# Kernel tuning notes

Measured on AMD Instinct MI355X. Metric: run time of the kernel, lower is better.

## Reference

```python
import jax, jax.numpy as jnp
import numpy as np

N_HEADS = 16
NEG_BIAS = -1e9


def setup_inputs() -> dict:
    key = jax.random.key(0)
    kq, kk, kv = jax.random.split(key, 3)
    B, S, D = 2, 2048, 1024
    queries = jax.random.normal(kq, (B, S, D), dtype=jnp.float32)
    keys = jax.random.normal(kk, (B, S, D), dtype=jnp.float32)
    values = jax.random.normal(kv, (B, S, D), dtype=jnp.float32)
    # causal mask [B, S, S]: True = attend allowed
    mask = jnp.broadcast_to(jnp.tril(jnp.ones((S, S), dtype=bool)), (B, S, S))
    return {"queries": queries, "keys": keys, "values": values, "mask": mask}


def reference(queries, keys, values, mask):
    B, S, D = queries.shape
    H = N_HEADS
    dh = D // H

    def split_heads(t):  # [B,S,D] -> [B,H,S,dh]
        return t.reshape(B, -1, H, dh).transpose(0, 2, 1, 3)

    q = split_heads(queries)
    k = split_heads(keys)
    v = split_heads(values)

    # scaled dot-product similarity: [B,H,Sq,Sk]
    sim = jnp.einsum('bhqd,bhkd->bhqk', q, k) / jnp.sqrt(jnp.asarray(dh, q.dtype))

    # additive mask bias (mask rank 3 -> broadcast over heads)
    bias = NEG_BIAS * (~mask).astype(sim.dtype)  # [B,Sq,Sk]
    masked = sim + bias[:, None, :, :]

    # stable softmax (original subtracts row max then softmaxes)
    weights = jax.nn.softmax(masked, axis=-1)

    # dropout is identity at inference (rate=None -> 0)
    out = jnp.einsum('bhqk,bhkd->bhqd', weights, v)

    # combine heads: [B,H,S,dh] -> [B,S,D]
    out = out.transpose(0, 2, 1, 3).reshape(B, S, D)
    return out
```

## Files before the change

### kernel.cpp

```cpp
#include <hip/hip_runtime.h>

#define B_ 2
#define S_ 2048
#define D_ 1024
#define H_ 16
#define DH 64
#define KB 64
#define SCALE_LOG2 0.18033688011112042f
#define THR 11.0f

typedef _Float16 f16x8 __attribute__((ext_vector_type(8)));
typedef _Float16 f16x4 __attribute__((ext_vector_type(4)));
typedef __fp16   h16x2 __attribute__((ext_vector_type(2)));
typedef float f32x4 __attribute__((ext_vector_type(4)));


__device__ __forceinline__ f16x8 cvt8(const float* x, float s) {
  f16x8 r;
#pragma unroll
  for (int i = 0; i < 4; ++i) {
    h16x2 p = __builtin_amdgcn_cvt_pkrtz(x[2*i] * s, x[2*i+1] * s);
    r[2*i] = (_Float16)p[0]; r[2*i+1] = (_Float16)p[1];
  }
  return r;
}

__global__ __launch_bounds__(256) void mha_fwd(
    const float* __restrict__ qg, const float* __restrict__ kg,
    const float* __restrict__ vg, float* __restrict__ out)
{
  __shared__ __align__(16) _Float16 lds_k[KB * DH];
  __shared__ __align__(16) _Float16 lds_v[DH * KB];

  int bx  = blockIdx.x;
  int xcd = bx & 7;
  int L   = bx >> 3;
  int bh  = xcd * 4 + (L & 3);
  int qb  = 31 - (L >> 2);
  int h = bh & 15;
  int b = bh >> 4;

  int tid  = threadIdx.x;
  int wid  = tid >> 6;
  int lane = tid & 63;
  int n    = lane & 15;
  int g    = lane >> 4;

  const float* qbase = qg + (size_t)b * S_ * D_ + h * DH;
  const float* kbase = kg + (size_t)b * S_ * D_ + h * DH;
  const float* vbase = vg + (size_t)b * S_ * D_ + h * DH;

  const int skey  = tid >> 2;
  const int spart = tid & 3;
  const int vdh   = tid & 63;
  const int vkq   = tid >> 6;

  float4 kf[4];
  float  vf[16];

  auto load_tile = [&](int kt) {
    const float* kp = kbase + (size_t)(kt * KB + skey) * D_ + spart * 16;
#pragma unroll
    for (int i = 0; i < 4; ++i) kf[i] = ((const float4*)kp)[i];
    const float* vp = vbase + (size_t)(kt * KB + vkq * 16) * D_ + vdh;
#pragma unroll
    for (int j = 0; j < 16; ++j) vf[j] = vp[(size_t)j * D_];
  };

  auto store_tile = [&]() {
    const float* kfl = (const float*)kf;
    f16x8 h0 = cvt8(kfl, 1.f), h1 = cvt8(kfl + 8, 1.f);
    int c0 = spart * 2;
    char* kb_ = (char*)lds_k;
    *(f16x8*)(kb_ + skey * 128 + (((c0    ) ^ (skey & 7)) << 4)) = h0;
    *(f16x8*)(kb_ + skey * 128 + (((c0 + 1) ^ (skey & 7)) << 4)) = h1;
    f16x8 v0 = cvt8(vf, 1.f), v1 = cvt8(vf + 8, 1.f);
    int kb8 = vkq * 2;
    _Float16* vt = lds_v + vdh * 64;
    *(f16x8*)(vt + (((kb8    ) ^ (vdh & 7)) << 3)) = v0;
    *(f16x8*)(vt + (((kb8 + 1) ^ (vdh & 7)) << 3)) = v1;
  };

  const int nkt  = qb + 1;
  const int qrow = qb * 64 + wid * 16;

  f16x8 bq[2];
  {
    const float* qp = qbase + (size_t)(qrow + n) * D_ + g * 8;
    float x[16];
#pragma unroll
    for (int c = 0; c < 2; ++c) {
      *(float4*)(x + 8*c)     = *(const float4*)(qp + c * 32);
      *(float4*)(x + 8*c + 4) = *(const float4*)(qp + c * 32 + 4);
    }
    bq[0] = cvt8(x, SCALE_LOG2);
    bq[1] = cvt8(x + 8, SCALE_LOG2);
  }

  f32x4 o_acc[4] = {};
  float m_run = 0.f, l_run = 0.f;

  load_tile(0);

  for (int kt = 0; kt < nkt; ++kt) {
    __syncthreads();
    store_tile();
    __syncthreads();
    if (kt + 1 < nkt) load_tile(kt + 1);

    __builtin_amdgcn_s_setprio(1);
    const char* kb_ = (const char*)lds_k;
    f32x4 sc[4] = {};
#pragma unroll
    for (int t = 0; t < 4; ++t) {
      int keyl = t * 16 + n;
#pragma unroll
      for (int c = 0; c < 2; ++c) {
        int off = keyl * 128 + (((c * 4 + g) ^ (keyl & 7)) << 4);
        f16x8 ak = *(f16x8*)(kb_ + off);
        sc[t] = __builtin_amdgcn_mfma_f32_16x16x32_f16(ak, bq[c], sc[t], 0, 0, 0);
      }
    }

    if (kt == nkt - 1) {
      int q = qrow + n;
#pragma unroll
      for (int t = 0; t < 4; ++t)
#pragma unroll
        for (int r = 0; r < 4; ++r) {
          int key = kt * KB + t * 16 + 4 * g + r;
          if (key > q) sc[t][r] = -1e30f;
        }
    }

    float mxt[4];
#pragma unroll
    for (int t = 0; t < 4; ++t)
      mxt[t] = fmaxf(fmaxf(sc[t][0], sc[t][1]), fmaxf(sc[t][2], sc[t][3]));
    float mx = fmaxf(fmaxf(mxt[0], mxt[1]), fmaxf(mxt[2], mxt[3]));
    mx = fmaxf(mx, __shfl_xor(mx, 16, 64));
    mx = fmaxf(mx, __shfl_xor(mx, 32, 64));

    float s = 0.f;
#pragma unroll
    for (int t = 0; t < 4; ++t) {
      f32x4 p = sc[t];
#pragma unroll
      for (int r = 0; r < 4; ++r) p[r] = exp2f(p[r] - m_run);
      sc[t] = p;
      s += (p[0] + p[1]) + (p[2] + p[3]);
    }

    if (!__all(mx <= m_run + THR)) {
      float mnew  = fmaxf(m_run, mx);
      float alpha = exp2f(m_run - mnew);
#pragma unroll
      for (int t = 0; t < 4; ++t)
#pragma unroll
        for (int r = 0; r < 4; ++r) sc[t][r] *= alpha;
      s *= alpha;
      l_run *= alpha;
      m_run = mnew;
      float ar[4];
#pragma unroll
      for (int r = 0; r < 4; ++r) ar[r] = __shfl(alpha, 4 * g + r, 64);
#pragma unroll
      for (int nt = 0; nt < 4; ++nt)
#pragma unroll
        for (int r = 0; r < 4; ++r) o_acc[nt][r] *= ar[r];
    }
    l_run += s;

    f16x4 pa[4];
#pragma unroll
    for (int u = 0; u < 4; ++u) {
      h16x2 p0 = __builtin_amdgcn_cvt_pkrtz(sc[u][0], sc[u][1]);
      h16x2 p1 = __builtin_amdgcn_cvt_pkrtz(sc[u][2], sc[u][3]);
      f16x4 p4;
      p4[0] = (_Float16)p0[0]; p4[1] = (_Float16)p0[1];
      p4[2] = (_Float16)p1[0]; p4[3] = (_Float16)p1[1];
      pa[u] = p4;
    }

#pragma unroll
    for (int u = 0; u < 4; ++u) {
#pragma unroll
      for (int nt = 0; nt < 4; ++nt) {
        int dhv = nt * 16 + n;
        int off = dhv * 64 + ((((2 * u + (g >> 1)) ^ (n & 7))) << 3) + ((g & 1) << 2);
        f16x4 bv = *(f16x4*)(lds_v + off);
        o_acc[nt] = __builtin_amdgcn_mfma_f32_16x16x16f16(pa[u], bv, o_acc[nt], 0, 0, 0);
      }
    }
    __builtin_amdgcn_s_setprio(0);
  }

  float lsum = l_run;
  lsum += __shfl_xor(lsum, 16, 64);
  lsum += __shfl_xor(lsum, 32, 64);
  float linv[4];
#pragma unroll
  for (int r = 0; r < 4; ++r) linv[r] = 1.0f / __shfl(lsum, 4 * g + r, 64);

  float* ob = out + ((size_t)b * S_ + qrow) * D_ + h * DH;
#pragma unroll
  for (int r = 0; r < 4; ++r) {
    float* op = ob + (size_t)(4 * g + r) * D_ + n;
#pragma unroll
    for (int nt = 0; nt < 4; ++nt)
      op[nt * 16] = o_acc[nt][r] * linv[r];
  }
}

extern "C" void kernel_launch(void* const* d_in, const int* in_sizes, int n_in,
                              void* d_out, int out_size, void* d_ws, size_t ws_size,
                              hipStream_t stream) {
  const float* q = (const float*)d_in[0];
  const float* k = (const float*)d_in[1];
  const float* v = (const float*)d_in[2];
  float* out = (float*)d_out;
  dim3 grid(1024);
  mha_fwd<<<grid, 256, 0, stream>>>(q, k, v, out);
}
```

Baseline: 154.4 us.

## Split long causal query blocks across key chunks with atomic-counter merge

Each query block's key range is cut into chunks of 8 tiles, so the grid grows from 1024 to 2560 blocks and the causal triangle's work is spread more evenly. Each chunk writes a partial output in fp16 plus its row max and sum to workspace. The last-arriving block, found with an atomic counter, merges the partials with a log-sum-exp rescale. This adds an extra counter-zeroing launch, workspace traffic and fp16 rounding of the partials. The original single-pass kernel is kept as a fallback when workspace is too small.

```diff
diff --git a/kernel.cpp b/kernel.cpp
--- a/kernel.cpp
+++ b/kernel.cpp
@@ -9,6 +9,11 @@
 #define SCALE_LOG2 0.18033688011112042f
 #define THR 11.0f
 
+#define CHUNK 8
+#define PSTRIDE 8704
+#define NSLOTS 2304
+#define WS_NEED (4096 + NSLOTS * PSTRIDE)
+
 typedef _Float16 f16x8 __attribute__((ext_vector_type(8)));
 typedef _Float16 f16x4 __attribute__((ext_vector_type(4)));
 typedef __fp16   h16x2 __attribute__((ext_vector_type(2)));
@@ -25,18 +30,29 @@
   return r;
 }
 
-__global__ __launch_bounds__(256) void mha_fwd(
+__global__ void zero_cnt(int* c) {
+  int i = blockIdx.x * 256 + threadIdx.x;
+  if (i < 1024) c[i] = 0;
+}
+
+__global__ __launch_bounds__(256) void mha_fwd_split(
     const float* __restrict__ qg, const float* __restrict__ kg,
-    const float* __restrict__ vg, float* __restrict__ out)
+    const float* __restrict__ vg, float* __restrict__ out,
+    char* __restrict__ wsp)
 {
   __shared__ __align__(16) _Float16 lds_k[KB * DH];
   __shared__ __align__(16) _Float16 lds_v[DH * KB];
+  __shared__ int s_last;
 
   int bx  = blockIdx.x;
-  int xcd = bx & 7;
-  int L   = bx >> 3;
-  int bh  = xcd * 4 + (L & 3);
-  int qb  = 31 - (L >> 2);
+  int L   = (bx & 7) * 320 + (bx >> 3);
+  int bh  = L / 80;
+  int idx = 79 - (L % 80);
+  int qb, ch, nch;
+  if (idx < 8)       { qb = idx;                 ch = 0;              nch = 1; }
+  else if (idx < 24) { qb = 8  + ((idx - 8) >> 1);  ch = (idx - 8) & 1;  nch = 2; }
+  else if (idx < 48) { qb = 16 + (idx - 24) / 3;    ch = (idx - 24) % 3; nch = 3; }
+  else               { qb = 24 + ((idx - 48) >> 2); ch = (idx - 48) & 3; nch = 4; }
   int h = bh & 15;
   int b = bh >> 4;
 
@@ -82,6 +98,8 @@
   };
 
   const int nkt  = qb + 1;
+  const int k0   = ch * CHUNK;
+  const int kend = min(k0 + CHUNK, nkt);
   const int qrow = qb * 64 + wid * 16;
 
   f16x8 bq[2];
@@ -100,13 +118,13 @@
   f32x4 o_acc[4] = {};
   float m_run = 0.f, l_run = 0.f;
 
-  load_tile(0);
-
-  for (int kt = 0; kt < nkt; ++kt) {
+  load_tile(k0);
+
+  for (int kt = k0; kt < kend; ++kt) {
     __syncthreads();
     store_tile();
     __syncthreads();
-    if (kt + 1 < nkt) load_tile(kt + 1);
+    if (kt + 1 < kend) load_tile(kt + 1);
 
     __builtin_amdgcn_s_setprio(1);
     const char* kb_ = (const char*)lds_k;
@@ -122,7 +140,7 @@
       }
     }
 
-    if (kt == nkt - 1) {
+    if (kt == qb) {
       int q = qrow + n;
 #pragma unroll
       for (int t = 0; t < 4; ++t)
@@ -202,6 +220,249 @@
 #pragma unroll
   for (int r = 0; r < 4; ++r) linv[r] = 1.0f / __shfl(lsum, 4 * g + r, 64);
 
+  if (nch == 1) {
+    float* ob = out + ((size_t)b * S_ + qrow) * D_ + h * DH;
+#pragma unroll
+    for (int r = 0; r < 4; ++r) {
+      float* op = ob + (size_t)(4 * g + r) * D_ + n;
+#pragma unroll
+      for (int nt = 0; nt < 4; ++nt)
+        op[nt * 16] = o_acc[nt][r] * linv[r];
+    }
+    return;
+  }
+
+  int off_q = (qb < 16) ? (qb - 8) * 2 : (qb < 24) ? 16 + (qb - 16) * 3 : 40 + (qb - 24) * 4;
+  int slot0 = bh * 72 + off_q;
+  char* pbase = wsp + 4096 + (size_t)(slot0 + ch) * PSTRIDE;
+  {
+    _Float16* Op = (_Float16*)pbase;
+#pragma unroll
+    for (int r = 0; r < 4; ++r) {
+      int prow = wid * 16 + 4 * g + r;
+#pragma unroll
+      for (int nt = 0; nt < 4; ++nt)
+        Op[prow * 64 + nt * 16 + n] = (_Float16)(o_acc[nt][r] * linv[r]);
+    }
+    if (lane < 16) {
+      *(float*)(pbase + 8192 + (wid * 16 + n) * 4) = m_run;
+      *(float*)(pbase + 8448 + (wid * 16 + n) * 4) = lsum;
+    }
+  }
+  __threadfence();
+  __syncthreads();
+  int* cnt = (int*)wsp + bh * 24 + (qb - 8);
+  if (tid == 0) s_last = (atomicAdd(cnt, 1) == nch - 1);
+  __syncthreads();
+  if (!s_last) return;
+  __threadfence();
+
+  {
+    const char* pb0 = wsp + 4096 + (size_t)slot0 * PSTRIDE;
+    int row = tid >> 2;
+    int c0  = (tid & 3) * 16;
+    float mi[4], li[4], M = -1e30f;
+    for (int i = 0; i < nch; ++i) {
+      const char* p = pb0 + (size_t)i * PSTRIDE;
+      mi[i] = *(const float*)(p + 8192 + row * 4);
+      li[i] = *(const float*)(p + 8448 + row * 4);
+      M = fmaxf(M, mi[i]);
+    }
+    float o[16];
+#pragma unroll
+    for (int j = 0; j < 16; ++j) o[j] = 0.f;
+    float wsum = 0.f;
+    for (int i = 0; i < nch; ++i) {
+      float w = li[i] * exp2f(mi[i] - M);
+      wsum += w;
+      const _Float16* Op = (const _Float16*)(pb0 + (size_t)i * PSTRIDE) + row * 64 + c0;
+#pragma unroll
+      for (int j = 0; j < 16; ++j) o[j] += w * (float)Op[j];
+    }
+    float inv = 1.0f / wsum;
+    float* op = out + ((size_t)b * S_ + qb * 64 + row) * D_ + h * DH + c0;
+#pragma unroll
+    for (int j = 0; j < 16; ++j) op[j] = o[j] * inv;
+  }
+}
+
+__global__ __launch_bounds__(256) void mha_fwd(
+    const float* __restrict__ qg, const float* __restrict__ kg,
+    const float* __restrict__ vg, float* __restrict__ out)
+{
+  __shared__ __align__(16) _Float16 lds_k[KB * DH];
+  __shared__ __align__(16) _Float16 lds_v[DH * KB];
+
+  int bx  = blockIdx.x;
+  int xcd = bx & 7;
+  int L   = bx >> 3;
+  int bh  = xcd * 4 + (L & 3);
+  int qb  = 31 - (L >> 2);
+  int h = bh & 15;
+  int b = bh >> 4;
+
+  int tid  = threadIdx.x;
+  int wid  = tid >> 6;
+  int lane = tid & 63;
+  int n    = lane & 15;
+  int g    = lane >> 4;
+
+  const float* qbase = qg + (size_t)b * S_ * D_ + h * DH;
+  const float* kbase = kg + (size_t)b * S_ * D_ + h * DH;
+  const float* vbase = vg + (size_t)b * S_ * D_ + h * DH;
+
+  const int skey  = tid >> 2;
+  const int spart = tid & 3;
+  const int vdh   = tid & 63;
+  const int vkq   = tid >> 6;
+
+  float4 kf[4];
+  float  vf[16];
+
+  auto load_tile = [&](int kt) {
+    const float* kp = kbase + (size_t)(kt * KB + skey) * D_ + spart * 16;
+#pragma unroll
+    for (int i = 0; i < 4; ++i) kf[i] = ((const float4*)kp)[i];
+    const float* vp = vbase + (size_t)(kt * KB + vkq * 16) * D_ + vdh;
+#pragma unroll
+    for (int j = 0; j < 16; ++j) vf[j] = vp[(size_t)j * D_];
+  };
+
+  auto store_tile = [&]() {
+    const float* kfl = (const float*)kf;
+    f16x8 h0 = cvt8(kfl, 1.f), h1 = cvt8(kfl + 8, 1.f);
+    int c0 = spart * 2;
+    char* kb_ = (char*)lds_k;
+    *(f16x8*)(kb_ + skey * 128 + (((c0    ) ^ (skey & 7)) << 4)) = h0;
+    *(f16x8*)(kb_ + skey * 128 + (((c0 + 1) ^ (skey & 7)) << 4)) = h1;
+    f16x8 v0 = cvt8(vf, 1.f), v1 = cvt8(vf + 8, 1.f);
+    int kb8 = vkq * 2;
+    _Float16* vt = lds_v + vdh * 64;
+    *(f16x8*)(vt + (((kb8    ) ^ (vdh & 7)) << 3)) = v0;
+    *(f16x8*)(vt + (((kb8 + 1) ^ (vdh & 7)) << 3)) = v1;
+  };
+
+  const int nkt  = qb + 1;
+  const int qrow = qb * 64 + wid * 16;
+
+  f16x8 bq[2];
+  {
+    const float* qp = qbase + (size_t)(qrow + n) * D_ + g * 8;
+    float x[16];
+#pragma unroll
+    for (int c = 0; c < 2; ++c) {
+      *(float4*)(x + 8*c)     = *(const float4*)(qp + c * 32);
+      *(float4*)(x + 8*c + 4) = *(const float4*)(qp + c * 32 + 4);
+    }
+    bq[0] = cvt8(x, SCALE_LOG2);
+    bq[1] = cvt8(x + 8, SCALE_LOG2);
+  }
+
+  f32x4 o_acc[4] = {};
+  float m_run = 0.f, l_run = 0.f;
+
+  load_tile(0);
+
+  for (int kt = 0; kt < nkt; ++kt) {
+    __syncthreads();
+    store_tile();
+    __syncthreads();
+    if (kt + 1 < nkt) load_tile(kt + 1);
+
+    __builtin_amdgcn_s_setprio(1);
+    const char* kb_ = (const char*)lds_k;
+    f32x4 sc[4] = {};
+#pragma unroll
+    for (int t = 0; t < 4; ++t) {
+      int keyl = t * 16 + n;
+#pragma unroll
+      for (int c = 0; c < 2; ++c) {
+        int off = keyl * 128 + (((c * 4 + g) ^ (keyl & 7)) << 4);
+        f16x8 ak = *(f16x8*)(kb_ + off);
+        sc[t] = __builtin_amdgcn_mfma_f32_16x16x32_f16(ak, bq[c], sc[t], 0, 0, 0);
+      }
+    }
+
+    if (kt == nkt - 1) {
+      int q = qrow + n;
+#pragma unroll
+      for (int t = 0; t < 4; ++t)
+#pragma unroll
+        for (int r = 0; r < 4; ++r) {
+          int key = kt * KB + t * 16 + 4 * g + r;
+          if (key > q) sc[t][r] = -1e30f;
+        }
+    }
+
+    float mxt[4];
+#pragma unroll
+    for (int t = 0; t < 4; ++t)
+      mxt[t] = fmaxf(fmaxf(sc[t][0], sc[t][1]), fmaxf(sc[t][2], sc[t][3]));
+    float mx = fmaxf(fmaxf(mxt[0], mxt[1]), fmaxf(mxt[2], mxt[3]));
+    mx = fmaxf(mx, __shfl_xor(mx, 16, 64));
+    mx = fmaxf(mx, __shfl_xor(mx, 32, 64));
+
+    float s = 0.f;
+#pragma unroll
+    for (int t = 0; t < 4; ++t) {
+      f32x4 p = sc[t];
+#pragma unroll
+      for (int r = 0; r < 4; ++r) p[r] = exp2f(p[r] - m_run);
+      sc[t] = p;
+      s += (p[0] + p[1]) + (p[2] + p[3]);
+    }
+
+    if (!__all(mx <= m_run + THR)) {
+      float mnew  = fmaxf(m_run, mx);
+      float alpha = exp2f(m_run - mnew);
+#pragma unroll
+      for (int t = 0; t < 4; ++t)
+#pragma unroll
+        for (int r = 0; r < 4; ++r) sc[t][r] *= alpha;
+      s *= alpha;
+      l_run *= alpha;
+      m_run = mnew;
+      float ar[4];
+#pragma unroll
+      for (int r = 0; r < 4; ++r) ar[r] = __shfl(alpha, 4 * g + r, 64);
+#pragma unroll
+      for (int nt = 0; nt < 4; ++nt)
+#pragma unroll
+        for (int r = 0; r < 4; ++r) o_acc[nt][r] *= ar[r];
+    }
+    l_run += s;
+
+    f16x4 pa[4];
+#pragma unroll
+    for (int u = 0; u < 4; ++u) {
+      h16x2 p0 = __builtin_amdgcn_cvt_pkrtz(sc[u][0], sc[u][1]);
+      h16x2 p1 = __builtin_amdgcn_cvt_pkrtz(sc[u][2], sc[u][3]);
+      f16x4 p4;
+      p4[0] = (_Float16)p0[0]; p4[1] = (_Float16)p0[1];
+      p4[2] = (_Float16)p1[0]; p4[3] = (_Float16)p1[1];
+      pa[u] = p4;
+    }
+
+#pragma unroll
+    for (int u = 0; u < 4; ++u) {
+#pragma unroll
+      for (int nt = 0; nt < 4; ++nt) {
+        int dhv = nt * 16 + n;
+        int off = dhv * 64 + ((((2 * u + (g >> 1)) ^ (n & 7))) << 3) + ((g & 1) << 2);
+        f16x4 bv = *(f16x4*)(lds_v + off);
+        o_acc[nt] = __builtin_amdgcn_mfma_f32_16x16x16f16(pa[u], bv, o_acc[nt], 0, 0, 0);
+      }
+    }
+    __builtin_amdgcn_s_setprio(0);
+  }
+
+  float lsum = l_run;
+  lsum += __shfl_xor(lsum, 16, 64);
+  lsum += __shfl_xor(lsum, 32, 64);
+  float linv[4];
+#pragma unroll
+  for (int r = 0; r < 4; ++r) linv[r] = 1.0f / __shfl(lsum, 4 * g + r, 64);
+
   float* ob = out + ((size_t)b * S_ + qrow) * D_ + h * DH;
 #pragma unroll
   for (int r = 0; r < 4; ++r) {
@@ -219,6 +480,10 @@
   const float* k = (const float*)d_in[1];
   const float* v = (const float*)d_in[2];
   float* out = (float*)d_out;
-  dim3 grid(1024);
-  mha_fwd<<<grid, 256, 0, stream>>>(q, k, v, out);
+  if (ws_size >= (size_t)WS_NEED) {
+    zero_cnt<<<4, 256, 0, stream>>>((int*)d_ws);
+    mha_fwd_split<<<2560, 256, 0, stream>>>(q, k, v, out, (char*)d_ws);
+  } else {
+    mha_fwd<<<1024, 256, 0, stream>>>(q, k, v, out);
+  }
 }
```

After: 559.2 us. +262.1%, slower.
